# Optimization experiments

Hardware: AMD Instinct MI355X
Metric: run time of the kernel (lower is better)

The kernel has to match this reference:

```python
import jax, jax.numpy as jnp
import numpy as np

N = 50000      # nodes
E = 800000     # edges (avg degree 16)
IN = 256       # in_feats
H = 4          # num_heads
D = 32         # out_feats per head
NEG_SLOPE = 0.2


def setup_inputs() -> dict:
    key = jax.random.key(0)
    k0, k1, k2, k3, k4, k5 = jax.random.split(key, 6)
    feat = jax.random.normal(k0, (N, IN), dtype=jnp.float32)
    src = jax.random.randint(k1, (E,), 0, N, dtype=jnp.int32)
    dst = jax.random.randint(k2, (E,), 0, N, dtype=jnp.int32)
    # fc weight [H*D, IN] (xavier-normal scale), attn vectors [H, D], bias [H*D]
    W = jax.random.normal(k3, (H * D, IN), dtype=jnp.float32) * np.float32(np.sqrt(2.0 / (IN + H * D)))
    attn_l = jax.random.normal(k4, (H, D), dtype=jnp.float32) * np.float32(np.sqrt(2.0 / (1 + D)))
    attn_r = jax.random.normal(k5, (H, D), dtype=jnp.float32) * np.float32(np.sqrt(2.0 / (1 + D)))
    bias = jnp.zeros((H * D,), dtype=jnp.float32)
    return {"feat": feat, "src": src, "dst": dst, "W": W,
            "attn_l": attn_l, "attn_r": attn_r, "bias": bias}


def reference(feat, src, dst, W, attn_l, attn_r, bias):
    # projection: [N, IN] @ [IN, H*D] -> [N, H, D]
    fh = (feat @ W.T).reshape(N, H, D)
    # per-node attention logits [N, H]
    el = jnp.einsum('nhd,hd->nh', fh, attn_l)
    er = jnp.einsum('nhd,hd->nh', fh, attn_r)
    # u_add_v edge scores [E, H] + LeakyReLU
    e = jax.nn.leaky_relu(el[src] + er[dst], negative_slope=NEG_SLOPE)
    # edge_softmax grouped by destination node (numerically stable)
    emax = jax.ops.segment_max(e, dst, num_segments=N)          # [N, H]
    ee = jnp.exp(e - emax[dst])                                  # [E, H]
    denom = jax.ops.segment_sum(ee, dst, num_segments=N)        # [N, H]
    a = ee / denom[dst]                                          # [E, H]
    # u_mul_e message + sum aggregation: [E, H, D] -> [N, H, D]
    m = fh[src] * a[:, :, None]
    rst = jax.ops.segment_sum(m, dst, num_segments=N)
    rst = rst + bias.reshape(1, H, D)
    return rst
```

## Files before the change

kernel.cpp:

```cpp
#include <hip/hip_runtime.h>
#include <math.h>

#define N_NODES 50000
#define N_EDGES 800000
#define IN_F    256
#define HD      128
#define NH      4
#define NEG     0.2f

#define SCAN_B  256
#define NB1     ((N_NODES + SCAN_B - 1) / SCAN_B)

typedef __attribute__((ext_vector_type(8))) short short8;
typedef __attribute__((ext_vector_type(4))) float f32x4;
typedef __attribute__((ext_vector_type(4))) unsigned int u32x4;

__device__ __forceinline__ float lrelu(float x) { return x > 0.f ? x : NEG * x; }

__global__ void k_init(int* __restrict__ deg, int* __restrict__ cursor) {
    int i = blockIdx.x * blockDim.x + threadIdx.x;
    if (i < N_NODES) { deg[i] = 0; cursor[i] = 0; }
}

__global__ void k_hist(const int* __restrict__ dst, int* __restrict__ deg) {
    int e = blockIdx.x * blockDim.x + threadIdx.x;
    if (e < N_EDGES) atomicAdd(&deg[dst[e]], 1);
}

__global__ void k_scan1(const int* __restrict__ deg, int* __restrict__ row_ptr,
                        int* __restrict__ bsum) {
    __shared__ int sm[SCAN_B];
    const int tid = threadIdx.x;
    const int t = blockIdx.x * SCAN_B + tid;
    int x = (t < N_NODES) ? deg[t] : 0;
    sm[tid] = x;
    __syncthreads();
#pragma unroll
    for (int off = 1; off < SCAN_B; off <<= 1) {
        int v = (tid >= off) ? sm[tid - off] : 0;
        __syncthreads();
        sm[tid] += v;
        __syncthreads();
    }
    if (t < N_NODES) row_ptr[t + 1] = sm[tid];
    if (tid == SCAN_B - 1) bsum[blockIdx.x] = sm[tid];
}

__global__ void k_scan2(const int* __restrict__ bsum, int* __restrict__ boff) {
    __shared__ int sm[SCAN_B];
    const int tid = threadIdx.x;
    int x = (tid < NB1) ? bsum[tid] : 0;
    sm[tid] = x;
    __syncthreads();
#pragma unroll
    for (int off = 1; off < SCAN_B; off <<= 1) {
        int v = (tid >= off) ? sm[tid - off] : 0;
        __syncthreads();
        sm[tid] += v;
        __syncthreads();
    }
    if (tid < NB1) boff[tid] = sm[tid] - x;
}

__global__ void k_scan3(int* __restrict__ row_ptr, const int* __restrict__ boff) {
    const int t = blockIdx.x * SCAN_B + threadIdx.x;
    if (t == 0) row_ptr[0] = 0;
    if (t < N_NODES) row_ptr[t + 1] += boff[blockIdx.x];
}

__global__ void k_scatter(const int* __restrict__ src, const int* __restrict__ dst,
                          const int* __restrict__ row_ptr, int* __restrict__ cursor,
                          int* __restrict__ sorted_src) {
    int e = blockIdx.x * blockDim.x + threadIdx.x;
    if (e >= N_EDGES) return;
    int d = dst[e];
    int slot = row_ptr[d] + atomicAdd(&cursor[d], 1);
    sorted_src[slot] = src[e];
}

#define BM 64
#define KP 40

__device__ __forceinline__ void split8(const float* __restrict__ p,
                                       unsigned* __restrict__ hu, unsigned* __restrict__ lu) {
    float v[8];
    *(float4*)(v)     = *(const float4*)(p);
    *(float4*)(v + 4) = *(const float4*)(p + 4);
#pragma unroll
    for (int j = 0; j < 4; ++j) {
        float a = v[2 * j], b = v[2 * j + 1];
        unsigned ha = __float_as_uint(a) >> 16;
        unsigned hb = __float_as_uint(b) >> 16;
        float ra = a - __uint_as_float(ha << 16);
        float rb = b - __uint_as_float(hb << 16);
        unsigned la = __float_as_uint(ra) >> 16;
        unsigned lb = __float_as_uint(rb) >> 16;
        hu[j] = ha | (hb << 16);
        lu[j] = la | (lb << 16);
    }
}

__launch_bounds__(256)
__global__ void k_gemm(const float* __restrict__ feat, const float* __restrict__ W,
                       float* __restrict__ fh) {
    __shared__ unsigned short Ah[BM][KP], Al[BM][KP];
    __shared__ unsigned short Bh[HD][KP], Bl[HD][KP];
    const int tid = threadIdx.x;
    const int w = tid >> 6;
    const int l = tid & 63;
    const int row0 = blockIdx.x * BM;

    f32x4 acc[8];
#pragma unroll
    for (int f = 0; f < 8; ++f) acc[f] = (f32x4)(0.f);

    const int ar = tid >> 2;
    const int ak = (tid & 3) << 3;
    const int br = tid >> 1;
    const int bk = (tid & 1) << 4;
    int agr = row0 + ar; if (agr >= N_NODES) agr = N_NODES - 1;
    const float* aptr = &feat[(size_t)agr * IN_F + ak];
    const float* bptr = &W[(size_t)br * IN_F + bk];

    const int fr = (w << 4) + (l & 15);
    const int fo = (l >> 4) << 3;

    for (int k0 = 0; k0 < IN_F; k0 += 32) {
        unsigned hua[4], lua[4], hb0[4], lb0[4], hb1[4], lb1[4];
        split8(aptr + k0, hua, lua);
        split8(bptr + k0, hb0, lb0);
        split8(bptr + k0 + 8, hb1, lb1);
        __syncthreads();
        *(u32x4*)&Ah[ar][ak]     = (u32x4){hua[0], hua[1], hua[2], hua[3]};
        *(u32x4*)&Al[ar][ak]     = (u32x4){lua[0], lua[1], lua[2], lua[3]};
        *(u32x4*)&Bh[br][bk]     = (u32x4){hb0[0], hb0[1], hb0[2], hb0[3]};
        *(u32x4*)&Bl[br][bk]     = (u32x4){lb0[0], lb0[1], lb0[2], lb0[3]};
        *(u32x4*)&Bh[br][bk + 8] = (u32x4){hb1[0], hb1[1], hb1[2], hb1[3]};
        *(u32x4*)&Bl[br][bk + 8] = (u32x4){lb1[0], lb1[1], lb1[2], lb1[3]};
        __syncthreads();

        short8 a_h = *(short8*)&Ah[fr][fo];
        short8 a_l = *(short8*)&Al[fr][fo];
#pragma unroll
        for (int f = 0; f < 8; ++f) {
            short8 b_h = *(short8*)&Bh[(f << 4) + (l & 15)][fo];
            short8 b_l = *(short8*)&Bl[(f << 4) + (l & 15)][fo];
            acc[f] = __builtin_amdgcn_mfma_f32_16x16x32_bf16(a_h, b_h, acc[f], 0, 0, 0);
            acc[f] = __builtin_amdgcn_mfma_f32_16x16x32_bf16(a_h, b_l, acc[f], 0, 0, 0);
            acc[f] = __builtin_amdgcn_mfma_f32_16x16x32_bf16(a_l, b_h, acc[f], 0, 0, 0);
        }
    }

    const int rbase = row0 + (w << 4) + ((l >> 4) << 2);
    const int col = l & 15;
#pragma unroll
    for (int f = 0; f < 8; ++f)
#pragma unroll
        for (int r = 0; r < 4; ++r) {
            int gr = rbase + r;
            if (gr < N_NODES)
                fh[(size_t)gr * HD + (f << 4) + col] = acc[f][r];
        }
}

__global__ void k_elr(const float* __restrict__ fh, const float* __restrict__ al,
                      const float* __restrict__ ar, float* __restrict__ el,
                      float* __restrict__ er) {
    const int tid = threadIdx.x;
    const int n = blockIdx.x * 2 + (tid >> 7);
    const int c = tid & 127;
    if (n >= N_NODES) return;
    float v = fh[(size_t)n * HD + c];
    float sl = v * al[c];
    float sr = v * ar[c];
#pragma unroll
    for (int off = 16; off >= 1; off >>= 1) {
        sl += __shfl_xor(sl, off, 32);
        sr += __shfl_xor(sr, off, 32);
    }
    if ((c & 31) == 0) {
        el[n * NH + (c >> 5)] = sl;
        er[n * NH + (c >> 5)] = sr;
    }
}

#define NPB 8
__launch_bounds__(256)
__global__ void k_node(const int* __restrict__ row_ptr, const int* __restrict__ sorted_src,
                       const float4* __restrict__ el4, const float4* __restrict__ er4,
                       const float4* __restrict__ fh4, const float4* __restrict__ bias4,
                       float4* __restrict__ out4) {
    __shared__ float lp[NPB][32 * 5];
    __shared__ int   lsrc[NPB][32];
    const int tid = threadIdx.x;
    const int g = tid >> 5;
    const int lane = tid & 31;
    const int n = blockIdx.x * NPB + g;
    if (n >= N_NODES) return;
    const int start = row_ptr[n], end = row_ptr[n + 1];
    const int h = lane >> 3;

    const float4 r4 = er4[n];
    float4 m = make_float4(-INFINITY, -INFINITY, -INFINITY, -INFINITY);
    float4 s = make_float4(0.f, 0.f, 0.f, 0.f);
    float4 acc = make_float4(0.f, 0.f, 0.f, 0.f);

    for (int chunk = start; chunk < end; chunk += 32) {
        const int e = chunk + lane;
        float4 sc = make_float4(-INFINITY, -INFINITY, -INFINITY, -INFINITY);
        int sidx = 0;
        if (e < end) {
            sidx = sorted_src[e];
            float4 l4 = el4[sidx];
            sc.x = lrelu(l4.x + r4.x);
            sc.y = lrelu(l4.y + r4.y);
            sc.z = lrelu(l4.z + r4.z);
            sc.w = lrelu(l4.w + r4.w);
        }
        float4 cm = sc;
#pragma unroll
        for (int off = 16; off >= 1; off >>= 1) {
            cm.x = fmaxf(cm.x, __shfl_xor(cm.x, off, 32));
            cm.y = fmaxf(cm.y, __shfl_xor(cm.y, off, 32));
            cm.z = fmaxf(cm.z, __shfl_xor(cm.z, off, 32));
            cm.w = fmaxf(cm.w, __shfl_xor(cm.w, off, 32));
        }
        float4 mn;
        mn.x = fmaxf(m.x, cm.x); mn.y = fmaxf(m.y, cm.y);
        mn.z = fmaxf(m.z, cm.z); mn.w = fmaxf(m.w, cm.w);
        float4 scale;
        scale.x = expf(m.x - mn.x); scale.y = expf(m.y - mn.y);
        scale.z = expf(m.z - mn.z); scale.w = expf(m.w - mn.w);
        m = mn;
        float4 p;
        p.x = expf(sc.x - mn.x); p.y = expf(sc.y - mn.y);
        p.z = expf(sc.z - mn.z); p.w = expf(sc.w - mn.w);
        float4 ps = p;
#pragma unroll
        for (int off = 16; off >= 1; off >>= 1) {
            ps.x += __shfl_xor(ps.x, off, 32);
            ps.y += __shfl_xor(ps.y, off, 32);
            ps.z += __shfl_xor(ps.z, off, 32);
            ps.w += __shfl_xor(ps.w, off, 32);
        }
        s.x = s.x * scale.x + ps.x;
        s.y = s.y * scale.y + ps.y;
        s.z = s.z * scale.z + ps.z;
        s.w = s.w * scale.w + ps.w;
        float sh = h == 0 ? scale.x : h == 1 ? scale.y : h == 2 ? scale.z : scale.w;
        acc.x *= sh; acc.y *= sh; acc.z *= sh; acc.w *= sh;

        lp[g][lane * 5 + 0] = p.x;
        lp[g][lane * 5 + 1] = p.y;
        lp[g][lane * 5 + 2] = p.z;
        lp[g][lane * 5 + 3] = p.w;
        lsrc[g][lane] = sidx;
        const int cnt = min(32, end - chunk);
        for (int j = 0; j < cnt; ++j) {
            float pj = lp[g][j * 5 + h];
            float4 v = fh4[(size_t)lsrc[g][j] * 32 + lane];
            acc.x += v.x * pj; acc.y += v.y * pj;
            acc.z += v.z * pj; acc.w += v.w * pj;
        }
    }
    float den = h == 0 ? s.x : h == 1 ? s.y : h == 2 ? s.z : s.w;
    float inv = den > 0.f ? 1.f / den : 0.f;
    float4 b = bias4[lane];
    float4 o;
    o.x = acc.x * inv + b.x; o.y = acc.y * inv + b.y;
    o.z = acc.z * inv + b.z; o.w = acc.w * inv + b.w;
    out4[(size_t)n * 32 + lane] = o;
}

extern "C" void kernel_launch(void* const* d_in, const int* in_sizes, int n_in,
                              void* d_out, int out_size, void* d_ws, size_t ws_size,
                              hipStream_t stream) {
    const float* feat   = (const float*)d_in[0];
    const int*   src    = (const int*)d_in[1];
    const int*   dst    = (const int*)d_in[2];
    const float* W      = (const float*)d_in[3];
    const float* attn_l = (const float*)d_in[4];
    const float* attn_r = (const float*)d_in[5];
    const float* bias   = (const float*)d_in[6];
    float* out = (float*)d_out;

    char* ws = (char*)d_ws;
    size_t off = 0;
    auto take = [&](size_t bytes) {
        char* p = ws + off;
        off = (off + bytes + 255) & ~(size_t)255;
        return p;
    };
    float* fh         = (float*)take((size_t)N_NODES * HD * 4);
    int*   sorted_src = (int*)take((size_t)N_EDGES * 4);
    float* el         = (float*)take((size_t)N_NODES * NH * 4);
    float* er         = (float*)take((size_t)N_NODES * NH * 4);
    int*   row_ptr    = (int*)take((size_t)(N_NODES + 1) * 4);
    int*   deg        = (int*)take((size_t)N_NODES * 4);
    int*   cursor     = (int*)take((size_t)N_NODES * 4);
    int*   bsum       = (int*)take((size_t)NB1 * 4);
    int*   boff       = (int*)take((size_t)NB1 * 4);
    (void)ws_size; (void)in_sizes; (void)n_in; (void)out_size;

    k_init<<<(N_NODES + 255) / 256, 256, 0, stream>>>(deg, cursor);
    k_hist<<<(N_EDGES + 255) / 256, 256, 0, stream>>>(dst, deg);
    k_scan1<<<NB1, SCAN_B, 0, stream>>>(deg, row_ptr, bsum);
    k_scan2<<<1, SCAN_B, 0, stream>>>(bsum, boff);
    k_scan3<<<NB1, SCAN_B, 0, stream>>>(row_ptr, boff);
    k_scatter<<<(N_EDGES + 255) / 256, 256, 0, stream>>>(src, dst, row_ptr, cursor, sorted_src);
    k_gemm<<<(N_NODES + BM - 1) / BM, 256, 0, stream>>>(feat, W, fh);
    k_elr<<<(N_NODES + 1) / 2, 256, 0, stream>>>(fh, attn_l, attn_r, el, er);
    k_node<<<(N_NODES + NPB - 1) / NPB, 256, 0, stream>>>(
        row_ptr, sorted_src, (const float4*)el, (const float4*)er,
        (const float4*)fh, (const float4*)bias, (float4*)out);
}
```

Measured before the change: 276.4 us.

## Store projected features as bf16 and fuse attention logits into GEMM epilogue

```diff
diff --git a/kernel.cpp b/kernel.cpp
--- a/kernel.cpp
+++ b/kernel.cpp
@@ -102,7 +102,9 @@
 
 __launch_bounds__(256)
 __global__ void k_gemm(const float* __restrict__ feat, const float* __restrict__ W,
-                       float* __restrict__ fh) {
+                       const float* __restrict__ gal, const float* __restrict__ gar,
+                       unsigned short* __restrict__ fhb,
+                       float* __restrict__ el, float* __restrict__ er) {
     __shared__ unsigned short Ah[BM][KP], Al[BM][KP];
     __shared__ unsigned short Bh[HD][KP], Bl[HD][KP];
     const int tid = threadIdx.x;
@@ -153,34 +155,56 @@
 
     const int rbase = row0 + (w << 4) + ((l >> 4) << 2);
     const int col = l & 15;
+
 #pragma unroll
     for (int f = 0; f < 8; ++f)
 #pragma unroll
         for (int r = 0; r < 4; ++r) {
             int gr = rbase + r;
-            if (gr < N_NODES)
-                fh[(size_t)gr * HD + (f << 4) + col] = acc[f][r];
-        }
-}
-
-__global__ void k_elr(const float* __restrict__ fh, const float* __restrict__ al,
-                      const float* __restrict__ ar, float* __restrict__ el,
-                      float* __restrict__ er) {
-    const int tid = threadIdx.x;
-    const int n = blockIdx.x * 2 + (tid >> 7);
-    const int c = tid & 127;
-    if (n >= N_NODES) return;
-    float v = fh[(size_t)n * HD + c];
-    float sl = v * al[c];
-    float sr = v * ar[c];
-#pragma unroll
-    for (int off = 16; off >= 1; off >>= 1) {
-        sl += __shfl_xor(sl, off, 32);
-        sr += __shfl_xor(sr, off, 32);
-    }
-    if ((c & 31) == 0) {
-        el[n * NH + (c >> 5)] = sl;
-        er[n * NH + (c >> 5)] = sr;
+            if (gr < N_NODES) {
+                unsigned u = __float_as_uint(acc[f][r]);
+                u += 0x7fffu + ((u >> 16) & 1u);
+                fhb[(size_t)gr * HD + (f << 4) + col] = (unsigned short)(u >> 16);
+            }
+        }
+
+    float pl[4][4], pr[4][4];
+#pragma unroll
+    for (int r = 0; r < 4; ++r)
+#pragma unroll
+        for (int h = 0; h < 4; ++h) { pl[r][h] = 0.f; pr[r][h] = 0.f; }
+#pragma unroll
+    for (int f = 0; f < 8; ++f) {
+        int c = (f << 4) + col;
+        float alc = gal[c], arc = gar[c];
+        int hh = f >> 1;
+#pragma unroll
+        for (int r = 0; r < 4; ++r) {
+            pl[r][hh] += acc[f][r] * alc;
+            pr[r][hh] += acc[f][r] * arc;
+        }
+    }
+#pragma unroll
+    for (int off = 8; off >= 1; off >>= 1)
+#pragma unroll
+        for (int r = 0; r < 4; ++r)
+#pragma unroll
+            for (int h = 0; h < 4; ++h) {
+                pl[r][h] += __shfl_xor(pl[r][h], off, 16);
+                pr[r][h] += __shfl_xor(pr[r][h], off, 16);
+            }
+    if (col == 0) {
+#pragma unroll
+        for (int r = 0; r < 4; ++r) {
+            int gr = rbase + r;
+            if (gr < N_NODES) {
+#pragma unroll
+                for (int h = 0; h < 4; ++h) {
+                    el[gr * NH + h] = pl[r][h];
+                    er[gr * NH + h] = pr[r][h];
+                }
+            }
+        }
     }
 }
 
@@ -188,8 +212,8 @@
 __launch_bounds__(256)
 __global__ void k_node(const int* __restrict__ row_ptr, const int* __restrict__ sorted_src,
                        const float4* __restrict__ el4, const float4* __restrict__ er4,
-                       const float4* __restrict__ fh4, const float4* __restrict__ bias4,
-                       float4* __restrict__ out4) {
+                       const unsigned short* __restrict__ fhb,
+                       const float4* __restrict__ bias4, float4* __restrict__ out4) {
     __shared__ float lp[NPB][32 * 5];
     __shared__ int   lsrc[NPB][32];
     const int tid = threadIdx.x;
@@ -198,12 +222,16 @@
     const int n = blockIdx.x * NPB + g;
     if (n >= N_NODES) return;
     const int start = row_ptr[n], end = row_ptr[n + 1];
-    const int h = lane >> 3;
+    const int half = lane >> 4;
+    const int cg   = lane & 15;
+    const int h2   = cg >> 2;
 
     const float4 r4 = er4[n];
     float4 m = make_float4(-INFINITY, -INFINITY, -INFINITY, -INFINITY);
     float4 s = make_float4(0.f, 0.f, 0.f, 0.f);
-    float4 acc = make_float4(0.f, 0.f, 0.f, 0.f);
+    float acc[8];
+#pragma unroll
+    for (int k = 0; k < 8; ++k) acc[k] = 0.f;
 
     for (int chunk = start; chunk < end; chunk += 32) {
         const int e = chunk + lane;
@@ -247,8 +275,9 @@
         s.y = s.y * scale.y + ps.y;
         s.z = s.z * scale.z + ps.z;
         s.w = s.w * scale.w + ps.w;
-        float sh = h == 0 ? scale.x : h == 1 ? scale.y : h == 2 ? scale.z : scale.w;
-        acc.x *= sh; acc.y *= sh; acc.z *= sh; acc.w *= sh;
+        float sh = h2 == 0 ? scale.x : h2 == 1 ? scale.y : h2 == 2 ? scale.z : scale.w;
+#pragma unroll
+        for (int k = 0; k < 8; ++k) acc[k] *= sh;
 
         lp[g][lane * 5 + 0] = p.x;
         lp[g][lane * 5 + 1] = p.y;
@@ -256,20 +285,39 @@
         lp[g][lane * 5 + 3] = p.w;
         lsrc[g][lane] = sidx;
         const int cnt = min(32, end - chunk);
-        for (int j = 0; j < cnt; ++j) {
-            float pj = lp[g][j * 5 + h];
-            float4 v = fh4[(size_t)lsrc[g][j] * 32 + lane];
-            acc.x += v.x * pj; acc.y += v.y * pj;
-            acc.z += v.z * pj; acc.w += v.w * pj;
-        }
-    }
-    float den = h == 0 ? s.x : h == 1 ? s.y : h == 2 ? s.z : s.w;
+        for (int j = 0; j < cnt; j += 2) {
+            const int jj = j + half;
+            const bool valid = jj < cnt;
+            const int jx = valid ? jj : 0;
+            float pj = lp[g][jx * 5 + h2];
+            if (!valid) pj = 0.f;
+            const int s2 = lsrc[g][jx];
+            u32x4 raw = *(const u32x4*)(fhb + (size_t)s2 * HD + cg * 8);
+#pragma unroll
+            for (int t = 0; t < 4; ++t) {
+                float lo = __uint_as_float(raw[t] << 16);
+                float hi = __uint_as_float(raw[t] & 0xffff0000u);
+                acc[2 * t]     += lo * pj;
+                acc[2 * t + 1] += hi * pj;
+            }
+        }
+    }
+#pragma unroll
+    for (int k = 0; k < 8; ++k) acc[k] += __shfl_xor(acc[k], 16, 32);
+
+    float den = h2 == 0 ? s.x : h2 == 1 ? s.y : h2 == 2 ? s.z : s.w;
     float inv = den > 0.f ? 1.f / den : 0.f;
-    float4 b = bias4[lane];
-    float4 o;
-    o.x = acc.x * inv + b.x; o.y = acc.y * inv + b.y;
-    o.z = acc.z * inv + b.z; o.w = acc.w * inv + b.w;
-    out4[(size_t)n * 32 + lane] = o;
+    if (half == 0) {
+        float4 b0 = bias4[cg * 2 + 0];
+        float4 b1 = bias4[cg * 2 + 1];
+        float4 o0, o1;
+        o0.x = acc[0] * inv + b0.x; o0.y = acc[1] * inv + b0.y;
+        o0.z = acc[2] * inv + b0.z; o0.w = acc[3] * inv + b0.w;
+        o1.x = acc[4] * inv + b1.x; o1.y = acc[5] * inv + b1.y;
+        o1.z = acc[6] * inv + b1.z; o1.w = acc[7] * inv + b1.w;
+        out4[(size_t)n * 32 + cg * 2 + 0] = o0;
+        out4[(size_t)n * 32 + cg * 2 + 1] = o1;
+    }
 }
 
 extern "C" void kernel_launch(void* const* d_in, const int* in_sizes, int n_in,
@@ -291,15 +339,15 @@
         off = (off + bytes + 255) & ~(size_t)255;
         return p;
     };
-    float* fh         = (float*)take((size_t)N_NODES * HD * 4);
-    int*   sorted_src = (int*)take((size_t)N_EDGES * 4);
-    float* el         = (float*)take((size_t)N_NODES * NH * 4);
-    float* er         = (float*)take((size_t)N_NODES * NH * 4);
-    int*   row_ptr    = (int*)take((size_t)(N_NODES + 1) * 4);
-    int*   deg        = (int*)take((size_t)N_NODES * 4);
-    int*   cursor     = (int*)take((size_t)N_NODES * 4);
-    int*   bsum       = (int*)take((size_t)NB1 * 4);
-    int*   boff       = (int*)take((size_t)NB1 * 4);
+    unsigned short* fhb = (unsigned short*)take((size_t)N_NODES * HD * 2);
+    int*   sorted_src   = (int*)take((size_t)N_EDGES * 4);
+    float* el           = (float*)take((size_t)N_NODES * NH * 4);
+    float* er           = (float*)take((size_t)N_NODES * NH * 4);
+    int*   row_ptr      = (int*)take((size_t)(N_NODES + 1) * 4);
+    int*   deg          = (int*)take((size_t)N_NODES * 4);
+    int*   cursor       = (int*)take((size_t)N_NODES * 4);
+    int*   bsum         = (int*)take((size_t)NB1 * 4);
+    int*   boff         = (int*)take((size_t)NB1 * 4);
     (void)ws_size; (void)in_sizes; (void)n_in; (void)out_size;
 
     k_init<<<(N_NODES + 255) / 256, 256, 0, stream>>>(deg, cursor);
@@ -308,9 +356,8 @@
     k_scan2<<<1, SCAN_B, 0, stream>>>(bsum, boff);
     k_scan3<<<NB1, SCAN_B, 0, stream>>>(row_ptr, boff);
     k_scatter<<<(N_EDGES + 255) / 256, 256, 0, stream>>>(src, dst, row_ptr, cursor, sorted_src);
-    k_gemm<<<(N_NODES + BM - 1) / BM, 256, 0, stream>>>(feat, W, fh);
-    k_elr<<<(N_NODES + 1) / 2, 256, 0, stream>>>(fh, attn_l, attn_r, el, er);
+    k_gemm<<<(N_NODES + BM - 1) / BM, 256, 0, stream>>>(feat, W, attn_l, attn_r, fhb, el, er);
     k_node<<<(N_NODES + NPB - 1) / NPB, 256, 0, stream>>>(
         row_ptr, sorted_src, (const float4*)el, (const float4*)er,
-        (const float4*)fh, (const float4*)bias, (float4*)out);
-}
+        fhb, (const float4*)bias, (float4*)out);
+}
```

After: 246.0 us. 11.0% less time.
